# Performance work log

Hardware: AMD Instinct MI355X
Metric: run time of the kernel (lower is better)

Reference implementation:

```python
import jax, jax.numpy as jnp
import numpy as np

NH, NKV, HD, ROPE_DIMS, ROPE_BASE = 16, 4, 128, 64, 10000.0


def _rms_norm(x):
    eps = jnp.asarray(jnp.finfo(x.dtype).eps, x.dtype)
    return x * jax.lax.rsqrt(jnp.mean(x * x, axis=-1, keepdims=True) + eps)


def _apply_rope_partial(x, cos, sin):
    # x: [B, H, T, hd]; cos/sin: [T, rope_dims//2]
    h = ROPE_DIMS // 2
    xa, xb, xp = x[..., :h], x[..., h:ROPE_DIMS], x[..., ROPE_DIMS:]
    c, s = cos[None, None], sin[None, None]
    rot = jnp.concatenate([xa * c - xb * s, xa * s + xb * c], axis=-1)
    return jnp.concatenate([rot, xp], axis=-1)


def setup_inputs() -> dict:
    key = jax.random.key(0)
    ks = jax.random.split(key, 7)
    B, T, D = 2, 2048, 2048
    kv_dim = NKV * HD
    sc = lambda n: 1.0 / np.sqrt(n)
    return {
        "x": jax.random.normal(ks[0], (B, T, D), jnp.float32),
        "ve_embed": jax.random.normal(ks[1], (B, T, kv_dim), jnp.float32),
        "Wq": jax.random.normal(ks[2], (D, D), jnp.float32) * sc(D),
        "Wk": jax.random.normal(ks[3], (kv_dim, D), jnp.float32) * sc(D),
        "Wv": jax.random.normal(ks[4], (kv_dim, D), jnp.float32) * sc(D),
        "Wproj": jax.random.normal(ks[5], (D, D), jnp.float32) * sc(D),
        "q_gain": jnp.full((NH,), 12.0, jnp.float32)
        + 0.01 * jax.random.normal(ks[6], (NH,), jnp.float32),
    }


def reference(x, ve_embed, Wq, Wk, Wv, Wproj, q_gain):
    B, T, D = x.shape
    g = NH // NKV  # GQA group size

    # QKV projections -> [B, H, T, hd]
    q = (x @ Wq.T).reshape(B, T, NH, HD).transpose(0, 2, 1, 3)
    k = (x @ Wk.T).reshape(B, T, NKV, HD).transpose(0, 2, 1, 3)
    v = (x @ Wv.T).reshape(B, T, NKV, HD).transpose(0, 2, 1, 3)

    q, k = _rms_norm(q), _rms_norm(k)

    # partial RoPE (frequencies built over full hd, first rope_dims//2 used)
    inv_freq = 1.0 / ROPE_BASE ** (jnp.arange(0, HD, 2, dtype=jnp.float32) / HD)
    f = jnp.arange(T, dtype=jnp.float32)[:, None] * inv_freq[None, :]  # [T, hd//2]
    cos, sin = jnp.cos(f)[:, : ROPE_DIMS // 2], jnp.sin(f)[:, : ROPE_DIMS // 2]
    q = _apply_rope_partial(q, cos, sin)
    k = _apply_rope_partial(k, cos, sin)

    q = q * q_gain[None, :, None, None]
    v = v + ve_embed.reshape(B, T, NKV, HD).transpose(0, 2, 1, 3)

    # GQA causal attention: q grouped as [B, nkv, g, T, hd]
    qg = q.reshape(B, NKV, g, T, HD)
    scale = 1.0 / np.sqrt(HD)
    scores = jnp.einsum("bkgtd,bksd->bkgts", qg, k) * scale
    causal = jnp.tril(jnp.ones((T, T), bool))
    scores = jnp.where(causal[None, None, None], scores, -jnp.inf)
    p = jax.nn.softmax(scores, axis=-1)
    y = jnp.einsum("bkgts,bksd->bkgtd", p, v)  # [B, nkv, g, T, hd]

    y = y.reshape(B, NH, T, HD).transpose(0, 2, 1, 3).reshape(B, T, D)
    return y @ Wproj.T
```

## Files before the change

kernel.cpp:

```cpp
#include <hip/hip_runtime.h>
#include <hip/hip_bf16.h>
#include <cstdint>
#include <cstddef>


typedef _Float16 f16_t;
typedef f16_t f16x4 __attribute__((ext_vector_type(4)));
typedef f16_t f16x8 __attribute__((ext_vector_type(8)));
typedef float f32x4 __attribute__((ext_vector_type(4)));

#define MFMA16F(a, b, c) __builtin_amdgcn_mfma_f32_16x16x32_f16((a), (b), (c), 0, 0, 0)
#define SBAR()   __builtin_amdgcn_s_barrier()
#define SCHED0() __builtin_amdgcn_sched_barrier(0)
#define LGKM0()  asm volatile("s_waitcnt lgkmcnt(0)" ::: "memory")

__device__ __forceinline__ void gload16(const f16_t* g, f16_t* l) {
  auto lds_ptr = reinterpret_cast<__attribute__((address_space(3))) unsigned int*>(
      reinterpret_cast<uintptr_t>(l));
  auto g_ptr = reinterpret_cast<const __attribute__((address_space(1))) unsigned int*>(
      reinterpret_cast<uintptr_t>(g));
  __builtin_amdgcn_global_load_lds(g_ptr, lds_ptr, 16, 0, 0);
}

__device__ __forceinline__ void cast4(const float* __restrict__ s, f16_t* __restrict__ d) {
  const float4 v = *reinterpret_cast<const float4*>(s);
  f16_t r[4] = {(f16_t)v.x, (f16_t)v.y, (f16_t)v.z, (f16_t)v.w};
  *reinterpret_cast<uint64_t*>(d) = *reinterpret_cast<const uint64_t*>(r);
}

__global__ __launch_bounds__(256) void k_prep(
    const float* __restrict__ x, const float* __restrict__ Wq,
    const float* __restrict__ Wk, const float* __restrict__ Wv,
    const float* __restrict__ Wp, f16_t* __restrict__ xf,
    f16_t* __restrict__ wqkvf, f16_t* __restrict__ wpf,
    float* __restrict__ ctab, float* __restrict__ stab)
{
  const long N4X = 2097152;
  const long N4W = 1572864;
  const long N4P = 1048576;
  const long N4R = 16384;
  long i = (long)blockIdx.x * blockDim.x + threadIdx.x;
  const long step = (long)gridDim.x * blockDim.x;
  for (; i < N4X + N4W + N4P + N4R; i += step) {
    if (i < N4X) {
      cast4(x + i * 4, xf + i * 4);
    } else if (i < N4X + N4W) {
      const long j = (i - N4X) * 4;
      const long row = j >> 11, col = j & 2047;
      const float* src = (row < 2048) ? (Wq + row * 2048)
                       : (row < 2560) ? (Wk + (row - 2048) * 2048)
                                      : (Wv + (row - 2560) * 2048);
      cast4(src + col, wqkvf + j);
    } else if (i < N4X + N4W + N4P) {
      const long j = (i - N4X - N4W) * 4;
      cast4(Wp + j, wpf + j);
    } else {
      const long j = (i - N4X - N4W - N4P) * 4;
#pragma unroll
      for (int k = 0; k < 4; ++k) {
        const long idx = j + k;
        const int t = (int)(idx >> 5), fi = (int)(idx & 31);
        const float freq = exp2f(-(float)fi * 0.2076205059304601f);
        const float f = (float)t * freq;
        ctab[idx] = cosf(f);
        stab[idx] = sinf(f);
      }
    }
  }
}

__global__ __launch_bounds__(256) void k_vtrans(
    const f16_t* __restrict__ vn, f16_t* __restrict__ vt)
{
  __shared__ __align__(16) f16_t lsT[64 * 136];
  const int t0 = blockIdx.x * 64;
  const int bk = blockIdx.y;
  const f16_t* src = vn + ((size_t)bk * 2048 + t0) * 128;
  f16_t* dst = vt + (size_t)bk * 128 * 2048;
  const int tid = threadIdx.x;
#pragma unroll
  for (int it = 0; it < 4; ++it) {
    const int cch = tid + it * 256;
    const int r = cch >> 4, c = cch & 15;
    *reinterpret_cast<f16x8*>(&lsT[r * 136 + c * 8]) =
        *reinterpret_cast<const f16x8*>(src + (size_t)r * 128 + c * 8);
  }
  __syncthreads();
#pragma unroll
  for (int it = 0; it < 4; ++it) {
    const int u = tid + it * 256;
    const int d = u >> 3, c8 = u & 7;
    f16_t vals[8];
#pragma unroll
    for (int j = 0; j < 8; ++j) vals[j] = lsT[(c8 * 8 + j) * 136 + d];
    *reinterpret_cast<f16x8*>(dst + (size_t)d * 2048 + t0 + c8 * 8) =
        *reinterpret_cast<const f16x8*>(vals);
  }
}

template <int NBU, typename OutT>
__global__ __launch_bounds__(1024, 1) void k_gemmQ(
    const f16_t* __restrict__ A, const f16_t* __restrict__ Bm,
    OutT* __restrict__ C, int M, int N, int K, int lda, int ldb)
{
  __shared__ __align__(16) f16_t lds[2][(4 + NBU) * 4096];
  const int tid = threadIdx.x;
  const int l = tid & 63, w = tid >> 6;
  const int lrow = l & 15, lk = l >> 4;
  const int wm = w >> 2, wn = w & 3;

  const int nwg = gridDim.x * gridDim.y;
  int lin = blockIdx.y * gridDim.x + blockIdx.x;
  lin = (lin & 7) * (nwg >> 3) + (lin >> 3);
  const int m0 = (lin / gridDim.x) * 256, n0 = (lin % gridDim.x) * (64 * NBU);

  const bool stager = (tid < 512);
  const int srow = tid >> 3;
  const int scol = ((tid & 7) ^ (srow & 7)) << 3;
  const f16_t* gP[4 + NBU];
#pragma unroll
  for (int u = 0; u < 4; ++u) gP[u] = A + (size_t)(m0 + u * 64 + srow) * lda + scol;
#pragma unroll
  for (int u = 0; u < NBU; ++u) gP[4 + u] = Bm + (size_t)(n0 + u * 64 + srow) * ldb + scol;

  auto stageAll = [&](int buf, int k0) {
#pragma unroll
    for (int u = 0; u < 4 + NBU; ++u)
      gload16(gP[u] + k0, &lds[buf][u * 4096 + tid * 8]);
  };
  auto rdA = [&](int buf, int mf, int ks) -> f16x8 {
    const int row = wm * 64 + mf * 16 + lrow;
    const int slot = ((ks << 2) | lk) ^ (row & 7);
    return *reinterpret_cast<const f16x8*>(&lds[buf][row * 64 + slot * 8]);
  };
  auto rdB = [&](int buf, int nf, int ks) -> f16x8 {
    const int row = wn * (16 * NBU) + nf * 16 + lrow;
    const int slot = ((ks << 2) | lk) ^ (row & 7);
    return *reinterpret_cast<const f16x8*>(&lds[buf][16384 + row * 64 + slot * 8]);
  };

  f32x4 acc[4][NBU] = {};
  const int nkt = K >> 6;

  if (stager) {
    stageAll(0, 0);
    stageAll(1, nkt > 1 ? 64 : 0);
  }
  if constexpr (NBU == 3) { asm volatile("s_waitcnt vmcnt(7)" ::: "memory"); }
  else                    { asm volatile("s_waitcnt vmcnt(6)" ::: "memory"); }
  SCHED0();
  SBAR(); SCHED0();

  f16x8 aA[4][2], bB[NBU][2];
  for (int kt = 0; kt < nkt; ++kt) {
    const int b = kt & 1;
    const int kn2 = (kt + 2 < nkt ? kt + 2 : nkt - 1) << 6;

#pragma unroll
    for (int mf = 0; mf < 4; ++mf) { aA[mf][0] = rdA(b, mf, 0); aA[mf][1] = rdA(b, mf, 1); }
#pragma unroll
    for (int nf = 0; nf < NBU; ++nf) { bB[nf][0] = rdB(b, nf, 0); bB[nf][1] = rdB(b, nf, 1); }
    __builtin_amdgcn_s_setprio(1);
#pragma unroll
    for (int mf = 0; mf < 2; ++mf)
#pragma unroll
      for (int nf = 0; nf < NBU; ++nf)
#pragma unroll
        for (int ks = 0; ks < 2; ++ks)
          acc[mf][nf] = MFMA16F(aA[mf][ks], bB[nf][ks], acc[mf][nf]);
    __builtin_amdgcn_s_setprio(0);
    LGKM0(); SCHED0();
    SBAR(); SCHED0();

    if (stager) stageAll(b, kn2);
    if constexpr (NBU == 3) { asm volatile("s_waitcnt vmcnt(7)" ::: "memory"); }
    else                    { asm volatile("s_waitcnt vmcnt(6)" ::: "memory"); }
    SCHED0();
    __builtin_amdgcn_s_setprio(1);
#pragma unroll
    for (int mf = 2; mf < 4; ++mf)
#pragma unroll
      for (int nf = 0; nf < NBU; ++nf)
#pragma unroll
        for (int ks = 0; ks < 2; ++ks)
          acc[mf][nf] = MFMA16F(aA[mf][ks], bB[nf][ks], acc[mf][nf]);
    __builtin_amdgcn_s_setprio(0);
    SBAR(); SCHED0();
  }

#pragma unroll
  for (int mf = 0; mf < 4; ++mf) {
    const int row = m0 + wm * 64 + mf * 16 + lk * 4;
#pragma unroll
    for (int nf = 0; nf < NBU; ++nf) {
      const int col = n0 + wn * (16 * NBU) + nf * 16 + lrow;
#pragma unroll
      for (int rg = 0; rg < 4; ++rg)
        C[(size_t)(row + rg) * N + col] = (OutT)acc[mf][nf][rg];
    }
  }
  (void)M;
}

__global__ __launch_bounds__(256) void k_qkv_epi(
    const f16_t* __restrict__ qkv, const float* __restrict__ ve,
    const float* __restrict__ qgain,
    const float* __restrict__ ctab, const float* __restrict__ stab,
    f16_t* __restrict__ qn, f16_t* __restrict__ kn, f16_t* __restrict__ vn)
{
  const int blk = blockIdx.x;
  const int b = blk >> 11, t = blk & 2047;
  const int w = threadIdx.x >> 6, l = threadIdx.x & 63;
  const int i32 = l & 31;
  const float c = ctab[t * 32 + i32], s = stab[t * 32 + i32];
  const float EPS = 1.1920929e-07f;
  constexpr float SCALE_L2E = 0.088388347648318447f * 1.4426950408889634f;

#pragma unroll
  for (int it = 0; it < 4; ++it) {
    const int h = w + it * 4;
    const f16_t* row = qkv + (size_t)blk * 3072 + h * 128;
    float x0 = (float)row[l], x1 = (float)row[l + 64];
    float ss = x0 * x0 + x1 * x1;
#pragma unroll
    for (int off = 32; off; off >>= 1) ss += __shfl_xor(ss, off);
    const float rn = rsqrtf(ss * (1.0f / 128.0f) + EPS);
    x0 *= rn; x1 *= rn;
    const float p = __shfl_xor(x0, 32);
    float xr = (l < 32) ? (x0 * c - p * s) : (p * s + x0 * c);
    const float g = qgain[h] * SCALE_L2E;
    xr *= g; x1 *= g;
    f16_t* orow = qn + (((size_t)(b * 16 + h)) * 2048 + t) * 128;
    orow[l] = (f16_t)xr;
    orow[l + 64] = (f16_t)x1;
  }
  {
    const f16_t* row = qkv + (size_t)blk * 3072 + 2048 + w * 128;
    float x0 = (float)row[l], x1 = (float)row[l + 64];
    float ss = x0 * x0 + x1 * x1;
#pragma unroll
    for (int off = 32; off; off >>= 1) ss += __shfl_xor(ss, off);
    const float rn = rsqrtf(ss * (1.0f / 128.0f) + EPS);
    x0 *= rn; x1 *= rn;
    const float p = __shfl_xor(x0, 32);
    const float xr = (l < 32) ? (x0 * c - p * s) : (p * s + x0 * c);
    f16_t* orow = kn + (((size_t)(b * 4 + w)) * 2048 + t) * 128;
    orow[l] = (f16_t)xr;
    orow[l + 64] = (f16_t)x1;
  }
  {
    const f16_t* row = qkv + (size_t)blk * 3072 + 2560 + w * 128;
    const float* verow = ve + (size_t)blk * 512 + w * 128;
    f16_t* orow = vn + (((size_t)(b * 4 + w)) * 2048 + t) * 128;
    orow[l] = (f16_t)((float)row[l] + verow[l]);
    orow[l + 64] = (f16_t)((float)row[l + 64] + verow[l + 64]);
  }
}

__global__ __launch_bounds__(256, 3) void k_attn(
    const f16_t* __restrict__ qn, const f16_t* __restrict__ kn,
    const f16_t* __restrict__ vt, f16_t* __restrict__ y,
    f16_t* __restrict__ po, float* __restrict__ pm, float* __restrict__ pl)
{
  __shared__ __align__(16) f16_t lsK[64 * 128];
  __shared__ __align__(16) f16_t lsV[128 * 64];
  __shared__ __align__(16) f16_t lsPb[4][16 * 64];
  const int j = blockIdx.y;
  int qt, sp, tstart, tcnt;
  bool split;
  if (j < 32) {
    qt = 31 - (j >> 1); sp = j & 1; split = true;
    const int tot = qt + 1, c0 = (tot + 1) >> 1;
    tstart = sp ? c0 : 0;
    tcnt = sp ? tot - c0 : c0;
  } else {
    qt = 47 - j; sp = 0; split = false; tstart = 0; tcnt = qt + 1;
  }
  const int bh = blockIdx.x;
  const int b = bh >> 4, h = bh & 15, kvh = h >> 2;
  const int tid = threadIdx.x, w = tid >> 6, l = tid & 63;
  const int lrow = l & 15, lk = l >> 4;
  const int qbase = qt * 64 + w * 16;
  constexpr float NEG = -1e30f;
  f16_t* lsP = lsPb[w];

  const f16_t* qp = qn + ((size_t)(b * 16 + h) * 2048) * 128;
  f16x8 aQ[4];
#pragma unroll
  for (int kf = 0; kf < 4; ++kf)
    aQ[kf] = *reinterpret_cast<const f16x8*>(
        qp + (size_t)(qbase + lrow) * 128 + kf * 32 + lk * 8);

  const f16_t* kp = kn + ((size_t)(b * 4 + kvh) * 2048) * 128;
  const f16_t* vtp = vt + (size_t)(b * 4 + kvh) * 128 * 2048;

  f32x4 o[8] = {};
  float mst = NEG;
  float lst = 0.f;

  f16x8 kreg[4], vreg[4];
  auto loadKV = [&](int t0) {
#pragma unroll
    for (int it = 0; it < 4; ++it) {
      const int cch = tid + it * 256;
      kreg[it] = *reinterpret_cast<const f16x8*>(
          kp + (size_t)(t0 + (cch >> 4)) * 128 + (cch & 15) * 8);
      vreg[it] = *reinterpret_cast<const f16x8*>(
          vtp + (size_t)(cch >> 3) * 2048 + t0 + (cch & 7) * 8);
    }
  };
  loadKV(tstart * 64);

  for (int ti = 0; ti < tcnt; ++ti) {
    const int tt = tstart + ti;
    __syncthreads();
#pragma unroll
    for (int it = 0; it < 4; ++it) {
      const int cch = tid + it * 256;
      const int r = cch >> 4, dg = cch & 15;
      *reinterpret_cast<f16x8*>(&lsK[r * 128 + ((dg ^ (r & 7)) << 3)]) = kreg[it];
      const int d = cch >> 3, c8 = cch & 7;
      *reinterpret_cast<f16x8*>(&lsV[d * 64 + ((c8 ^ (d & 7)) << 3)]) = vreg[it];
    }
    if (ti + 1 < tcnt) loadKV((tt + 1) * 64);
    __syncthreads();

    f32x4 sacc[4] = {};
#pragma unroll
    for (int cf = 0; cf < 4; ++cf) {
      const int krow = cf * 16 + lrow;
#pragma unroll
      for (int kf = 0; kf < 4; ++kf) {
        const f16x8 aK = *reinterpret_cast<const f16x8*>(
            &lsK[krow * 128 + ((((kf << 2) | lk) ^ (krow & 7)) << 3)]);
        sacc[cf] = MFMA16F(aK, aQ[kf], sacc[cf]);
      }
    }

    if (tt == qt) {
      const int qin = w * 16 + lrow;
#pragma unroll
      for (int cf = 0; cf < 4; ++cf)
#pragma unroll
        for (int rg = 0; rg < 4; ++rg)
          if (cf * 16 + lk * 4 + rg > qin) sacc[cf][rg] = NEG;
    }

    float mx = NEG;
#pragma unroll
    for (int cf = 0; cf < 4; ++cf)
      mx = fmaxf(mx, fmaxf(fmaxf(sacc[cf][0], sacc[cf][1]),
                           fmaxf(sacc[cf][2], sacc[cf][3])));
    if (__any(mx > mst + 8.f)) {
      float rmx = mx;
      rmx = fmaxf(rmx, __shfl_xor(rmx, 16));
      rmx = fmaxf(rmx, __shfl_xor(rmx, 32));
      const float mnew = fmaxf(mst, rmx);
      const float alpha = exp2f(mst - mnew);
      mst = mnew;
      lst *= alpha;
#pragma unroll
      for (int rg = 0; rg < 4; ++rg) {
        const float arow = __shfl(alpha, lk * 4 + rg);
#pragma unroll
        for (int df = 0; df < 8; ++df) o[df][rg] *= arow;
      }
    }
#pragma unroll
    for (int cf = 0; cf < 4; ++cf) {
#pragma unroll
      for (int rg = 0; rg < 4; ++rg) {
        const float p = exp2f(sacc[cf][rg] - mst);
        sacc[cf][rg] = p;
        lst += p;
      }
    }

#pragma unroll
    for (int cf = 0; cf < 4; ++cf) {
      f16x4 pk;
#pragma unroll
      for (int rg = 0; rg < 4; ++rg) pk[rg] = (f16_t)sacc[cf][rg];
      const int slot8 = cf * 2 + (lk >> 1);
      *reinterpret_cast<f16x4*>(
          &lsP[lrow * 64 + ((slot8 ^ (lrow & 7)) << 3) + (lk & 1) * 4]) = pk;
    }
#pragma unroll
    for (int k2 = 0; k2 < 2; ++k2) {
      const f16x8 aP = *reinterpret_cast<const f16x8*>(
          &lsP[lrow * 64 + ((((k2 << 2) | lk) ^ (lrow & 7)) << 3)]);
#pragma unroll
      for (int df = 0; df < 8; ++df) {
        const int row = df * 16 + lrow;
        const f16x8 bV = *reinterpret_cast<const f16x8*>(
            &lsV[row * 64 + ((((k2 << 2) | lk) ^ (row & 7)) << 3)]);
        o[df] = MFMA16F(aP, bV, o[df]);
      }
    }
  }

  lst += __shfl_xor(lst, 16);
  lst += __shfl_xor(lst, 32);

  if (!split) {
#pragma unroll
    for (int rg = 0; rg < 4; ++rg) {
      const float lrow_sum = __shfl(lst, lk * 4 + rg);
      const float inv = 1.0f / lrow_sum;
      const int qi = qbase + lk * 4 + rg;
      const size_t rowoff = ((size_t)(b * 2048 + qi)) * 2048 + h * 128;
#pragma unroll
      for (int df = 0; df < 8; ++df)
        y[rowoff + df * 16 + lrow] = (f16_t)(o[df][rg] * inv);
    }
  } else {
    const size_t jb = (((size_t)(sp * 2 + b) * 16 + h) * 1024);
#pragma unroll
    for (int rg = 0; rg < 4; ++rg) {
      const int qi = qbase + lk * 4 + rg;
      f16_t* prow = po + (jb + (qi - 1024)) * 128;
#pragma unroll
      for (int df = 0; df < 8; ++df)
        prow[df * 16 + lrow] = (f16_t)o[df][rg];
    }
    if (lk == 0) {
      const int qi = qbase + lrow;
      pm[jb + (qi - 1024)] = mst;
      pl[jb + (qi - 1024)] = lst;
    }
  }
}

__global__ __launch_bounds__(256) void k_combine(
    const f16_t* __restrict__ po, const float* __restrict__ pm,
    const float* __restrict__ pl, f16_t* __restrict__ y)
{
  const int bh = blockIdx.x;
  const int b = bh >> 4, h = bh & 15;
  const int tid = threadIdx.x;
  const int r = blockIdx.y * 32 + (tid >> 3);
  const int d0 = (tid & 7) * 16;
  const size_t base1 = (((size_t)(0 * 2 + b) * 16 + h) * 1024 + r);
  const size_t base2 = (((size_t)(1 * 2 + b) * 16 + h) * 1024 + r);
  const float m1 = pm[base1], m2 = pm[base2];
  const float l1 = pl[base1], l2 = pl[base2];
  const float m = fmaxf(m1, m2);
  const float f1 = exp2f(m1 - m), f2 = exp2f(m2 - m);
  const float inv = 1.0f / (f1 * l1 + f2 * l2);
  const f16_t* o1 = po + base1 * 128 + d0;
  const f16_t* o2 = po + base2 * 128 + d0;
  f16_t* yr = y + ((size_t)(b * 2048 + 1024 + r)) * 2048 + h * 128 + d0;
#pragma unroll
  for (int v = 0; v < 2; ++v) {
    const f16x8 a = *reinterpret_cast<const f16x8*>(o1 + v * 8);
    const f16x8 c = *reinterpret_cast<const f16x8*>(o2 + v * 8);
    f16_t outv[8];
#pragma unroll
    for (int jj = 0; jj < 8; ++jj)
      outv[jj] = (f16_t)((f1 * (float)a[jj] + f2 * (float)c[jj]) * inv);
    *reinterpret_cast<f16x8*>(yr + v * 8) = *reinterpret_cast<const f16x8*>(outv);
  }
}

extern "C" void kernel_launch(void* const* d_in, const int* in_sizes, int n_in,
                              void* d_out, int out_size, void* d_ws, size_t ws_size,
                              hipStream_t stream) {
  const float* x  = (const float*)d_in[0];
  const float* ve = (const float*)d_in[1];
  const float* Wq = (const float*)d_in[2];
  const float* Wk = (const float*)d_in[3];
  const float* Wv = (const float*)d_in[4];
  const float* Wp = (const float*)d_in[5];
  const float* qg = (const float*)d_in[6];
  float* out = (float*)d_out;

  char* ws = (char*)d_ws;
  size_t off = 0;
  auto alloc = [&](size_t bytes) -> char* {
    char* p = ws + off;
    off += (bytes + 255) & ~(size_t)255;
    return p;
  };

  f16_t* xf    = (f16_t*)alloc((size_t)4096 * 2048 * 2);
  f16_t* wqkvf = (f16_t*)alloc((size_t)3072 * 2048 * 2);
  f16_t* wpf   = (f16_t*)alloc((size_t)2048 * 2048 * 2);
  f16_t* qkvf  = (f16_t*)alloc((size_t)4096 * 3072 * 2);
  f16_t* kn    = (f16_t*)alloc((size_t)2 * 4 * 2048 * 128 * 2);
  f16_t* vn    = (f16_t*)alloc((size_t)2 * 4 * 2048 * 128 * 2);
  f16_t* vt    = (f16_t*)alloc((size_t)2 * 4 * 128 * 2048 * 2);
  f16_t* po    = (f16_t*)alloc((size_t)2 * 2 * 16 * 1024 * 128 * 2);
  float* pm    = (float*)alloc((size_t)2 * 2 * 16 * 1024 * 4);
  float* pl    = (float*)alloc((size_t)2 * 2 * 16 * 1024 * 4);
  float* ctab  = (float*)alloc((size_t)2048 * 32 * 4);
  float* stab  = (float*)alloc((size_t)2048 * 32 * 4);
  f16_t* qn    = xf;
  f16_t* yb    = qkvf;
  (void)ws_size; (void)in_sizes; (void)n_in; (void)out_size;

  k_prep<<<2048, 256, 0, stream>>>(x, Wq, Wk, Wv, Wp, xf, wqkvf, wpf, ctab, stab);

  k_gemmQ<3, f16_t><<<dim3(16, 16), 1024, 0, stream>>>(
      xf, wqkvf, qkvf, 4096, 3072, 2048, 2048, 2048);

  k_qkv_epi<<<4096, 256, 0, stream>>>(qkvf, ve, qg, ctab, stab, qn, kn, vn);

  k_vtrans<<<dim3(32, 8), 256, 0, stream>>>(vn, vt);

  k_attn<<<dim3(32, 48), 256, 0, stream>>>(qn, kn, vt, yb, po, pm, pl);

  k_combine<<<dim3(32, 32), 256, 0, stream>>>(po, pm, pl, yb);

  k_gemmQ<2, float><<<dim3(16, 16), 1024, 0, stream>>>(
      yb, wpf, out, 4096, 2048, 2048, 2048, 2048);
}
```

Before: 192.0 us.

## Double query tile per attention block to reuse K/V tiles across more rows

The attention kernel now handles 128 query rows per block instead of 64, with each wave owning two 16-row query fragments that share each K and V LDS read. This halves the number of K/V tile loads per query row and halves the grid, reworks the causal split scheduling, and lets waves with no valid keys skip the last diagonal tile. MFMA sections are wrapped in s_setprio. In exchange register pressure roughly doubles for accumulators, occupancy is lowered to 2 blocks per CU, and there are fewer blocks to balance the causal work.

After: 206.5 us. +7.5%, slower.

```diff
diff --git a/kernel.cpp b/kernel.cpp
--- a/kernel.cpp
+++ b/kernel.cpp
@@ -257,46 +257,46 @@
   }
 }
 
-__global__ __launch_bounds__(256, 3) void k_attn(
+__global__ __launch_bounds__(256, 2) void k_attn(
     const f16_t* __restrict__ qn, const f16_t* __restrict__ kn,
     const f16_t* __restrict__ vt, f16_t* __restrict__ y,
     f16_t* __restrict__ po, float* __restrict__ pm, float* __restrict__ pl)
 {
   __shared__ __align__(16) f16_t lsK[64 * 128];
   __shared__ __align__(16) f16_t lsV[128 * 64];
-  __shared__ __align__(16) f16_t lsPb[4][16 * 64];
+  __shared__ __align__(16) f16_t lsPb[4][2][16 * 64];
   const int j = blockIdx.y;
   int qt, sp, tstart, tcnt;
   bool split;
-  if (j < 32) {
-    qt = 31 - (j >> 1); sp = j & 1; split = true;
-    const int tot = qt + 1, c0 = (tot + 1) >> 1;
+  if (j < 16) {
+    qt = 15 - (j >> 1); sp = j & 1; split = true;
+    const int tot = 2 * qt + 2, c0 = qt + 1;
     tstart = sp ? c0 : 0;
     tcnt = sp ? tot - c0 : c0;
   } else {
-    qt = 47 - j; sp = 0; split = false; tstart = 0; tcnt = qt + 1;
+    qt = 23 - j; sp = 0; split = false; tstart = 0; tcnt = 2 * qt + 2;
   }
   const int bh = blockIdx.x;
   const int b = bh >> 4, h = bh & 15, kvh = h >> 2;
   const int tid = threadIdx.x, w = tid >> 6, l = tid & 63;
   const int lrow = l & 15, lk = l >> 4;
-  const int qbase = qt * 64 + w * 16;
+  const int qbase = qt * 128 + w * 32;
   constexpr float NEG = -1e30f;
-  f16_t* lsP = lsPb[w];
 
   const f16_t* qp = qn + ((size_t)(b * 16 + h) * 2048) * 128;
-  f16x8 aQ[4];
-#pragma unroll
-  for (int kf = 0; kf < 4; ++kf)
-    aQ[kf] = *reinterpret_cast<const f16x8*>(
-        qp + (size_t)(qbase + lrow) * 128 + kf * 32 + lk * 8);
+  f16x8 bQ[2][4];
+#pragma unroll
+  for (int qf = 0; qf < 2; ++qf)
+#pragma unroll
+    for (int kf = 0; kf < 4; ++kf)
+      bQ[qf][kf] = *reinterpret_cast<const f16x8*>(
+          qp + (size_t)(qbase + qf * 16 + lrow) * 128 + kf * 32 + lk * 8);
 
   const f16_t* kp = kn + ((size_t)(b * 4 + kvh) * 2048) * 128;
   const f16_t* vtp = vt + (size_t)(b * 4 + kvh) * 128 * 2048;
 
-  f32x4 o[8] = {};
-  float mst = NEG;
-  float lst = 0.f;
+  f32x4 o0[8] = {}, o1[8] = {};
+  float mst0 = NEG, mst1 = NEG, lst0 = 0.f, lst1 = 0.f;
 
   f16x8 kreg[4], vreg[4];
   auto loadKV = [&](int t0) {
@@ -325,7 +325,10 @@
     if (ti + 1 < tcnt) loadKV((tt + 1) * 64);
     __syncthreads();
 
-    f32x4 sacc[4] = {};
+    if (tt == 2 * qt + 1 && w < 2) continue;
+
+    f32x4 sacc0[4] = {}, sacc1[4] = {};
+    __builtin_amdgcn_s_setprio(1);
 #pragma unroll
     for (int cf = 0; cf < 4; ++cf) {
       const int krow = cf * 16 + lrow;
@@ -333,100 +336,128 @@
       for (int kf = 0; kf < 4; ++kf) {
         const f16x8 aK = *reinterpret_cast<const f16x8*>(
             &lsK[krow * 128 + ((((kf << 2) | lk) ^ (krow & 7)) << 3)]);
-        sacc[cf] = MFMA16F(aK, aQ[kf], sacc[cf]);
-      }
-    }
-
-    if (tt == qt) {
-      const int qin = w * 16 + lrow;
+        sacc0[cf] = MFMA16F(aK, bQ[0][kf], sacc0[cf]);
+        sacc1[cf] = MFMA16F(aK, bQ[1][kf], sacc1[cf]);
+      }
+    }
+    __builtin_amdgcn_s_setprio(0);
+
+    if (tt >= 2 * qt) {
+      const int kvoff = (tt - 2 * qt) * 64;
 #pragma unroll
       for (int cf = 0; cf < 4; ++cf)
 #pragma unroll
-        for (int rg = 0; rg < 4; ++rg)
-          if (cf * 16 + lk * 4 + rg > qin) sacc[cf][rg] = NEG;
-    }
-
-    float mx = NEG;
-#pragma unroll
-    for (int cf = 0; cf < 4; ++cf)
-      mx = fmaxf(mx, fmaxf(fmaxf(sacc[cf][0], sacc[cf][1]),
-                           fmaxf(sacc[cf][2], sacc[cf][3])));
-    if (__any(mx > mst + 8.f)) {
-      float rmx = mx;
-      rmx = fmaxf(rmx, __shfl_xor(rmx, 16));
-      rmx = fmaxf(rmx, __shfl_xor(rmx, 32));
-      const float mnew = fmaxf(mst, rmx);
-      const float alpha = exp2f(mst - mnew);
-      mst = mnew;
-      lst *= alpha;
-#pragma unroll
-      for (int rg = 0; rg < 4; ++rg) {
-        const float arow = __shfl(alpha, lk * 4 + rg);
-#pragma unroll
-        for (int df = 0; df < 8; ++df) o[df][rg] *= arow;
-      }
-    }
-#pragma unroll
-    for (int cf = 0; cf < 4; ++cf) {
-#pragma unroll
-      for (int rg = 0; rg < 4; ++rg) {
-        const float p = exp2f(sacc[cf][rg] - mst);
-        sacc[cf][rg] = p;
-        lst += p;
-      }
-    }
-
-#pragma unroll
-    for (int cf = 0; cf < 4; ++cf) {
-      f16x4 pk;
-#pragma unroll
-      for (int rg = 0; rg < 4; ++rg) pk[rg] = (f16_t)sacc[cf][rg];
-      const int slot8 = cf * 2 + (lk >> 1);
-      *reinterpret_cast<f16x4*>(
-          &lsP[lrow * 64 + ((slot8 ^ (lrow & 7)) << 3) + (lk & 1) * 4]) = pk;
-    }
+        for (int rg = 0; rg < 4; ++rg) {
+          const int kvl = kvoff + cf * 16 + lk * 4 + rg;
+          if (kvl > w * 32 + lrow) sacc0[cf][rg] = NEG;
+          if (kvl > w * 32 + 16 + lrow) sacc1[cf][rg] = NEG;
+        }
+    }
+
+#pragma unroll
+    for (int qf = 0; qf < 2; ++qf) {
+      f32x4* sacc = qf ? sacc1 : sacc0;
+      float& mst = qf ? mst1 : mst0;
+      float& lst = qf ? lst1 : lst0;
+      f32x4* o = qf ? o1 : o0;
+
+      float mx = NEG;
+#pragma unroll
+      for (int cf = 0; cf < 4; ++cf)
+        mx = fmaxf(mx, fmaxf(fmaxf(sacc[cf][0], sacc[cf][1]),
+                             fmaxf(sacc[cf][2], sacc[cf][3])));
+      if (__any(mx > mst + 8.f)) {
+        float rmx = mx;
+        rmx = fmaxf(rmx, __shfl_xor(rmx, 16));
+        rmx = fmaxf(rmx, __shfl_xor(rmx, 32));
+        const float mnew = fmaxf(mst, rmx);
+        const float alpha = exp2f(mst - mnew);
+        mst = mnew;
+        lst *= alpha;
+#pragma unroll
+        for (int rg = 0; rg < 4; ++rg) {
+          const float arow = __shfl(alpha, lk * 4 + rg);
+#pragma unroll
+          for (int df = 0; df < 8; ++df) o[df][rg] *= arow;
+        }
+      }
+#pragma unroll
+      for (int cf = 0; cf < 4; ++cf) {
+#pragma unroll
+        for (int rg = 0; rg < 4; ++rg) {
+          const float p = exp2f(sacc[cf][rg] - mst);
+          sacc[cf][rg] = p;
+          lst += p;
+        }
+      }
+#pragma unroll
+      for (int cf = 0; cf < 4; ++cf) {
+        f16x4 pk;
+#pragma unroll
+        for (int rg = 0; rg < 4; ++rg) pk[rg] = (f16_t)sacc[cf][rg];
+        const int slot8 = cf * 2 + (lk >> 1);
+        *reinterpret_cast<f16x4*>(
+            &lsPb[w][qf][lrow * 64 + ((slot8 ^ (lrow & 7)) << 3) + (lk & 1) * 4]) = pk;
+      }
+    }
+
+    __builtin_amdgcn_s_setprio(1);
 #pragma unroll
     for (int k2 = 0; k2 < 2; ++k2) {
-      const f16x8 aP = *reinterpret_cast<const f16x8*>(
-          &lsP[lrow * 64 + ((((k2 << 2) | lk) ^ (lrow & 7)) << 3)]);
+      const int pofs = lrow * 64 + ((((k2 << 2) | lk) ^ (lrow & 7)) << 3);
+      const f16x8 aP0 = *reinterpret_cast<const f16x8*>(&lsPb[w][0][pofs]);
+      const f16x8 aP1 = *reinterpret_cast<const f16x8*>(&lsPb[w][1][pofs]);
 #pragma unroll
       for (int df = 0; df < 8; ++df) {
         const int row = df * 16 + lrow;
         const f16x8 bV = *reinterpret_cast<const f16x8*>(
             &lsV[row * 64 + ((((k2 << 2) | lk) ^ (row & 7)) << 3)]);
-        o[df] = MFMA16F(aP, bV, o[df]);
-      }
-    }
-  }
-
-  lst += __shfl_xor(lst, 16);
-  lst += __shfl_xor(lst, 32);
+        o0[df] = MFMA16F(aP0, bV, o0[df]);
+        o1[df] = MFMA16F(aP1, bV, o1[df]);
+      }
+    }
+    __builtin_amdgcn_s_setprio(0);
+  }
+
+  lst0 += __shfl_xor(lst0, 16);
+  lst0 += __shfl_xor(lst0, 32);
+  lst1 += __shfl_xor(lst1, 16);
+  lst1 += __shfl_xor(lst1, 32);
 
   if (!split) {
 #pragma unroll
-    for (int rg = 0; rg < 4; ++rg) {
-      const float lrow_sum = __shfl(lst, lk * 4 + rg);
-      const float inv = 1.0f / lrow_sum;
-      const int qi = qbase + lk * 4 + rg;
-      const size_t rowoff = ((size_t)(b * 2048 + qi)) * 2048 + h * 128;
-#pragma unroll
-      for (int df = 0; df < 8; ++df)
-        y[rowoff + df * 16 + lrow] = (f16_t)(o[df][rg] * inv);
+    for (int qf = 0; qf < 2; ++qf) {
+      const f32x4* o = qf ? o1 : o0;
+      const float lstq = qf ? lst1 : lst0;
+#pragma unroll
+      for (int rg = 0; rg < 4; ++rg) {
+        const float lrow_sum = __shfl(lstq, lk * 4 + rg);
+        const float inv = 1.0f / lrow_sum;
+        const int qi = qbase + qf * 16 + lk * 4 + rg;
+        const size_t rowoff = ((size_t)(b * 2048 + qi)) * 2048 + h * 128;
+#pragma unroll
+        for (int df = 0; df < 8; ++df)
+          y[rowoff + df * 16 + lrow] = (f16_t)(o[df][rg] * inv);
+      }
     }
   } else {
     const size_t jb = (((size_t)(sp * 2 + b) * 16 + h) * 1024);
 #pragma unroll
-    for (int rg = 0; rg < 4; ++rg) {
-      const int qi = qbase + lk * 4 + rg;
-      f16_t* prow = po + (jb + (qi - 1024)) * 128;
-#pragma unroll
-      for (int df = 0; df < 8; ++df)
-        prow[df * 16 + lrow] = (f16_t)o[df][rg];
-    }
-    if (lk == 0) {
-      const int qi = qbase + lrow;
-      pm[jb + (qi - 1024)] = mst;
-      pl[jb + (qi - 1024)] = lst;
+    for (int qf = 0; qf < 2; ++qf) {
+      const f32x4* o = qf ? o1 : o0;
+#pragma unroll
+      for (int rg = 0; rg < 4; ++rg) {
+        const int qi = qbase + qf * 16 + lk * 4 + rg;
+        f16_t* prow = po + (jb + (qi - 1024)) * 128;
+#pragma unroll
+        for (int df = 0; df < 8; ++df)
+          prow[df * 16 + lrow] = (f16_t)o[df][rg];
+      }
+      if (lk == 0) {
+        const int qi = qbase + qf * 16 + lrow;
+        pm[jb + (qi - 1024)] = qf ? mst1 : mst0;
+        pl[jb + (qi - 1024)] = qf ? lst1 : lst0;
+      }
     }
   }
 }
@@ -507,7 +538,7 @@
 
   k_vtrans<<<dim3(32, 8), 256, 0, stream>>>(vn, vt);
 
-  k_attn<<<dim3(32, 48), 256, 0, stream>>>(qn, kn, vt, yb, po, pm, pl);
+  k_attn<<<dim3(32, 24), 256, 0, stream>>>(qn, kn, vt, yb, po, pm, pl);
 
   k_combine<<<dim3(32, 32), 256, 0, stream>>>(po, pm, pl, yb);
 
```
